# Kernel optimization log

Measured on AMD Instinct MI355X. Metric: run time of the kernel, lower is better.

The kernel has to match this reference:

```python
import jax, jax.numpy as jnp
import numpy as np

INPUT, HIDDEN, OUTPUT = 128, 256, 128
BATCH, SEQ = 128, 2048


def setup_inputs() -> dict:
    key = jax.random.key(0)
    ks = jax.random.split(key, 6)
    s_in = 1.0 / np.sqrt(INPUT)
    s_h = 1.0 / np.sqrt(HIDDEN)
    return {
        "x": jax.random.normal(ks[0], (BATCH, SEQ, INPUT), dtype=jnp.float32),
        "W_in": jax.random.uniform(ks[1], (HIDDEN, INPUT), jnp.float32, -s_in, s_in),
        "b_in": jax.random.uniform(ks[2], (HIDDEN,), jnp.float32, -s_in, s_in),
        "W_rec": jax.random.uniform(ks[3], (HIDDEN, HIDDEN), jnp.float32, -s_h, s_h),
        "W_out": jax.random.uniform(ks[4], (OUTPUT, HIDDEN), jnp.float32, -s_h, s_h),
        "b_out": jax.random.uniform(ks[5], (OUTPUT,), jnp.float32, -s_h, s_h),
    }


def reference(x, W_in, b_in, W_rec, W_out, b_out):
    # Precompute input projection for all timesteps in one big GEMM: [B,S,H]
    xin = jnp.einsum("bsi,hi->bsh", x, W_in) + b_in

    def step(h, xin_t):
        # h: [B,H]; xin_t: [B,H]
        h_new = jax.nn.sigmoid(xin_t + h @ W_rec.T)
        return h_new, None

    h0 = jnp.zeros((x.shape[0], W_rec.shape[0]), dtype=x.dtype)
    h_final, _ = jax.lax.scan(step, h0, jnp.swapaxes(xin, 0, 1))  # scan over seq
    return h_final @ W_out.T + b_out  # [B, OUTPUT]
```

## Files before the change

### kernel.cpp

```cpp
#include <hip/hip_runtime.h>
#include <hip/hip_bf16.h>


#define BATCH 128
#define SEQ   2048
#define NIN   128
#define NH    256
#define NOUT  128

#define BTILE 16
#define NBLK  (BATCH / BTILE)
#define HPITCH 264
#define XPITCH 136
#define TCHUNK 8
#define LOG2E 1.4426950408889634f

typedef __attribute__((ext_vector_type(8))) short short8;
typedef __attribute__((ext_vector_type(4))) float f32x4;

__device__ __forceinline__ ushort f2bf(float f) {
    union { float f; uint u; } v; v.f = f;
    uint r = v.u + 0x7fffu + ((v.u >> 16) & 1u);
    return (ushort)(r >> 16);
}

__device__ __forceinline__ uint pk_bf16(float a, float b) {
    float2 p; p.x = a; p.y = b;
    __hip_bfloat162 h = __float22bfloat162_rn(p);
    union { __hip_bfloat162 h; uint u; } v; v.h = h; return v.u;
}

__device__ __forceinline__ short8 load_wfrag_s(const float* __restrict__ W, int ld,
                                               int row, int col, float scale) {
    const float4* p = (const float4*)(W + (size_t)row * ld + col);
    float4 a = p[0], b = p[1];
    union { short8 v; ushort u[8]; } r;
    r.u[0] = f2bf(a.x * scale); r.u[1] = f2bf(a.y * scale);
    r.u[2] = f2bf(a.z * scale); r.u[3] = f2bf(a.w * scale);
    r.u[4] = f2bf(b.x * scale); r.u[5] = f2bf(b.y * scale);
    r.u[6] = f2bf(b.z * scale); r.u[7] = f2bf(b.w * scale);
    return r.v;
}

__device__ __forceinline__ float bfhi2f(uint u) {
    union { uint u; float f; } v; v.u = u & 0xffff0000u; return v.f;
}
__device__ __forceinline__ float bflo2f(uint u) {
    union { uint u; float f; } v; v.u = u << 16; return v.f;
}

__global__ __launch_bounds__(256, 2)
void xin_gemm(const float* __restrict__ x,
              const float* __restrict__ W_in,
              const float* __restrict__ b_in,
              uint2* __restrict__ xin) {
    const int tid  = threadIdx.x;
    const int lane = tid & 63;
    const int wid  = tid >> 6;
    const int n15  = lane & 15;
    const int q    = lane >> 4;
    const int bblk = blockIdx.x * BTILE;
    const int t0   = blockIdx.y * TCHUNK;

    short8 win[4][4];
    float  bias[4][4];
    #pragma unroll
    for (int mt = 0; mt < 4; ++mt) {
        const int row = (wid * 4 + mt) * 16 + n15;
        #pragma unroll
        for (int kt = 0; kt < 4; ++kt)
            win[mt][kt] = load_wfrag_s(W_in, NIN, row, kt * 32 + q * 8, LOG2E);
        #pragma unroll
        for (int r = 0; r < 4; ++r)
            bias[mt][r] = LOG2E * b_in[(wid * 4 + mt) * 16 + q * 4 + r];
    }

    const float* xrow = x + ((size_t)(bblk + n15) * SEQ + t0) * NIN + q * 8;

    #pragma unroll 1
    for (int tt = 0; tt < TCHUNK; ++tt) {
        const float* xp = xrow + (size_t)tt * NIN;
        short8 bx[4];
        #pragma unroll
        for (int kt = 0; kt < 4; ++kt) {
            const float4* p = (const float4*)(xp + kt * 32);
            float4 a = p[0], b = p[1];
            union { short8 v; uint u[4]; } r;
            r.u[0] = pk_bf16(a.x, a.y);
            r.u[1] = pk_bf16(a.z, a.w);
            r.u[2] = pk_bf16(b.x, b.y);
            r.u[3] = pk_bf16(b.z, b.w);
            bx[kt] = r.v;
        }
        f32x4 acc[4];
        #pragma unroll
        for (int mt = 0; mt < 4; ++mt) {
            acc[mt][0] = bias[mt][0]; acc[mt][1] = bias[mt][1];
            acc[mt][2] = bias[mt][2]; acc[mt][3] = bias[mt][3];
        }
        #pragma unroll
        for (int kt = 0; kt < 4; ++kt)
            #pragma unroll
            for (int mt = 0; mt < 4; ++mt)
                acc[mt] = __builtin_amdgcn_mfma_f32_16x16x32_bf16(
                    win[mt][kt], bx[kt], acc[mt], 0, 0, 0);

        const uint tb = ((uint)(t0 + tt) * NBLK + blockIdx.x) * 16u;
        #pragma unroll
        for (int mt = 0; mt < 4; ++mt) {
            uint2 w;
            w.x = pk_bf16(acc[mt][0], acc[mt][1]);
            w.y = pk_bf16(acc[mt][2], acc[mt][3]);
            xin[(size_t)((tb + wid * 4 + mt) * 64u + lane)] = w;
        }
    }
}

__global__ __launch_bounds__(512, 2)
void elman_scan(const uint2* __restrict__ xin,
                const float* __restrict__ W_rec,
                const float* __restrict__ W_out,
                const float* __restrict__ b_out,
                float* __restrict__ out) {
    const int tid  = threadIdx.x;
    const int lane = tid & 63;
    const int wid  = tid >> 6;
    const int n15  = lane & 15;
    const int q    = lane >> 4;
    const int bblk = blockIdx.x * BTILE;

    __shared__ __align__(16) uint2 hlds[2][16 * 64];

    short8 wrec[2][8];
    #pragma unroll
    for (int mt = 0; mt < 2; ++mt) {
        const int row = (wid * 2 + mt) * 16 + n15;
        #pragma unroll
        for (int kt = 0; kt < 8; ++kt)
            wrec[mt][kt] = load_wfrag_s(W_rec, NH, row, kt * 32 + q * 8, LOG2E);
    }

    for (int i = tid; i < 16 * 64; i += 512) {
        uint2 z; z.x = 0u; z.y = 0u;
        hlds[0][i] = z;
    }

    const uint loff = (uint)blockIdx.x * 1024u + (uint)(wid * 2) * 64u + (uint)lane;

    uint2 xa[2], xb[2];
    #pragma unroll
    for (int mt = 0; mt < 2; ++mt) xa[mt] = xin[(size_t)(loff + mt * 64u)];
    #pragma unroll
    for (int mt = 0; mt < 2; ++mt) xb[mt] = xin[(size_t)(8192u + loff + mt * 64u)];

    __syncthreads();

    const int rbase = n15 * 4 + 2 * (q & 1);
    const int shalf = q >> 1;
    const int woff  = n15 * 4 + q;

    auto step = [&](int t, uint2 (&X)[2]) {
        const int cur = t & 1, nxt = cur ^ 1;

        short8 bh[8];
        #pragma unroll
        for (int kt = 0; kt < 8; ++kt)
            bh[kt] = *(const short8*)&hlds[cur][(2 * kt + shalf) * 64 + rbase];

        f32x4 acc[2];
        #pragma unroll
        for (int mt = 0; mt < 2; ++mt) {
            acc[mt][0] = bflo2f(X[mt].x);
            acc[mt][1] = bfhi2f(X[mt].x);
            acc[mt][2] = bflo2f(X[mt].y);
            acc[mt][3] = bfhi2f(X[mt].y);
        }

        {
            const uint tp = (uint)((t + 2 < SEQ) ? (t + 2) : (SEQ - 1));
            const uint tb = tp * 8192u + loff;
            #pragma unroll
            for (int mt = 0; mt < 2; ++mt) X[mt] = xin[(size_t)(tb + mt * 64u)];
        }

        __builtin_amdgcn_s_setprio(1);
        #pragma unroll
        for (int kt = 0; kt < 8; ++kt)
            #pragma unroll
            for (int mt = 0; mt < 2; ++mt)
                acc[mt] = __builtin_amdgcn_mfma_f32_16x16x32_bf16(
                    wrec[mt][kt], bh[kt], acc[mt], 0, 0, 0);
        __builtin_amdgcn_s_setprio(0);

        #pragma unroll
        for (int mt = 0; mt < 2; ++mt) {
            float h0 = __builtin_amdgcn_rcpf(1.0f + __builtin_amdgcn_exp2f(-acc[mt][0]));
            float h1 = __builtin_amdgcn_rcpf(1.0f + __builtin_amdgcn_exp2f(-acc[mt][1]));
            float h2 = __builtin_amdgcn_rcpf(1.0f + __builtin_amdgcn_exp2f(-acc[mt][2]));
            float h3 = __builtin_amdgcn_rcpf(1.0f + __builtin_amdgcn_exp2f(-acc[mt][3]));
            uint2 w;
            w.x = pk_bf16(h0, h1);
            w.y = pk_bf16(h2, h3);
            hlds[nxt][(wid * 2 + mt) * 64 + woff] = w;
        }

        asm volatile("s_waitcnt lgkmcnt(0)" ::: "memory");
        __builtin_amdgcn_s_barrier();
    };

    #pragma unroll 1
    for (int t = 0; t < SEQ; t += 2) {
        step(t, xa);
        step(t + 1, xb);
    }

    short8 wout[8];
    float  bo[4];
    {
        const int row = wid * 16 + n15;
        #pragma unroll
        for (int kt = 0; kt < 8; ++kt)
            wout[kt] = load_wfrag_s(W_out, NH, row, kt * 32 + q * 8, 1.0f);
        #pragma unroll
        for (int r = 0; r < 4; ++r)
            bo[r] = b_out[wid * 16 + q * 4 + r];
    }
    f32x4 oacc;
    oacc[0] = bo[0]; oacc[1] = bo[1]; oacc[2] = bo[2]; oacc[3] = bo[3];
    #pragma unroll
    for (int kt = 0; kt < 8; ++kt) {
        short8 bh = *(const short8*)&hlds[0][(2 * kt + shalf) * 64 + rbase];
        oacc = __builtin_amdgcn_mfma_f32_16x16x32_bf16(wout[kt], bh, oacc, 0, 0, 0);
    }
    #pragma unroll
    for (int r = 0; r < 4; ++r) {
        const int o = wid * 16 + q * 4 + r;
        out[(size_t)(bblk + n15) * NOUT + o] = oacc[r];
    }
}

__global__ __launch_bounds__(256, 1)
void elman_mfma(const float* __restrict__ x,
                const float* __restrict__ W_in,
                const float* __restrict__ b_in,
                const float* __restrict__ W_rec,
                const float* __restrict__ W_out,
                const float* __restrict__ b_out,
                float* __restrict__ out) {
    const int tid  = threadIdx.x;
    const int lane = tid & 63;
    const int wid  = tid >> 6;
    const int n15  = lane & 15;
    const int q    = lane >> 4;
    const int bblk = blockIdx.x * BTILE;

    __shared__ __align__(16) ushort hlds[2][BTILE * HPITCH];
    __shared__ __align__(16) ushort xlds[2][BTILE * XPITCH];

    short8 wrec[4][8];
    short8 win[4][4];
    float  bias[4][4];
    #pragma unroll
    for (int mt = 0; mt < 4; ++mt) {
        const int row = (wid * 4 + mt) * 16 + n15;
        #pragma unroll
        for (int kt = 0; kt < 8; ++kt)
            wrec[mt][kt] = load_wfrag_s(W_rec, NH, row, kt * 32 + q * 8, 1.0f);
        #pragma unroll
        for (int kt = 0; kt < 4; ++kt)
            win[mt][kt] = load_wfrag_s(W_in, NIN, row, kt * 32 + q * 8, 1.0f);
        #pragma unroll
        for (int r = 0; r < 4; ++r)
            bias[mt][r] = b_in[(wid * 4 + mt) * 16 + q * 4 + r];
    }

    for (int i = tid; i < BTILE * HPITCH / 2; i += 256)
        ((uint*)hlds[0])[i] = 0u;

    const int xr = tid >> 4;
    const int xc = (tid & 15) * 8;
    const size_t xbase = ((size_t)(bblk + xr)) * SEQ * NIN + xc;
    {
        const float4* p = (const float4*)(x + xbase);
        float4 a = p[0], b = p[1];
        union { uint4 u4; ushort s[8]; } px;
        px.s[0] = f2bf(a.x); px.s[1] = f2bf(a.y); px.s[2] = f2bf(a.z); px.s[3] = f2bf(a.w);
        px.s[4] = f2bf(b.x); px.s[5] = f2bf(b.y); px.s[6] = f2bf(b.z); px.s[7] = f2bf(b.w);
        *(uint4*)&xlds[0][xr * XPITCH + xc] = px.u4;
    }
    __syncthreads();

    #pragma unroll 1
    for (int t = 0; t < SEQ; ++t) {
        const int cur = t & 1, nxt = cur ^ 1;
        float4 xp0{}, xp1{};
        if (t + 1 < SEQ) {
            const float4* p = (const float4*)(x + xbase + (size_t)(t + 1) * NIN);
            xp0 = p[0]; xp1 = p[1];
        }
        short8 bx[4], bh[8];
        #pragma unroll
        for (int kt = 0; kt < 4; ++kt)
            bx[kt] = *(const short8*)&xlds[cur][n15 * XPITCH + kt * 32 + q * 8];
        #pragma unroll
        for (int kt = 0; kt < 8; ++kt)
            bh[kt] = *(const short8*)&hlds[cur][n15 * HPITCH + kt * 32 + q * 8];
        f32x4 acc[4];
        #pragma unroll
        for (int mt = 0; mt < 4; ++mt) {
            acc[mt][0] = bias[mt][0]; acc[mt][1] = bias[mt][1];
            acc[mt][2] = bias[mt][2]; acc[mt][3] = bias[mt][3];
        }
        #pragma unroll
        for (int kt = 0; kt < 4; ++kt)
            #pragma unroll
            for (int mt = 0; mt < 4; ++mt)
                acc[mt] = __builtin_amdgcn_mfma_f32_16x16x32_bf16(
                    win[mt][kt], bx[kt], acc[mt], 0, 0, 0);
        #pragma unroll
        for (int kt = 0; kt < 8; ++kt)
            #pragma unroll
            for (int mt = 0; mt < 4; ++mt)
                acc[mt] = __builtin_amdgcn_mfma_f32_16x16x32_bf16(
                    wrec[mt][kt], bh[kt], acc[mt], 0, 0, 0);
        #pragma unroll
        for (int mt = 0; mt < 4; ++mt) {
            float h0 = 1.0f / (1.0f + __expf(-acc[mt][0]));
            float h1 = 1.0f / (1.0f + __expf(-acc[mt][1]));
            float h2 = 1.0f / (1.0f + __expf(-acc[mt][2]));
            float h3 = 1.0f / (1.0f + __expf(-acc[mt][3]));
            uint2 w;
            w.x = pk_bf16(h0, h1);
            w.y = pk_bf16(h2, h3);
            *(uint2*)&hlds[nxt][n15 * HPITCH + (wid * 4 + mt) * 16 + q * 4] = w;
        }
        if (t + 1 < SEQ) {
            union { uint4 u4; ushort s[8]; } px;
            px.s[0] = f2bf(xp0.x); px.s[1] = f2bf(xp0.y);
            px.s[2] = f2bf(xp0.z); px.s[3] = f2bf(xp0.w);
            px.s[4] = f2bf(xp1.x); px.s[5] = f2bf(xp1.y);
            px.s[6] = f2bf(xp1.z); px.s[7] = f2bf(xp1.w);
            *(uint4*)&xlds[nxt][xr * XPITCH + xc] = px.u4;
        }
        __syncthreads();
    }

    short8 wout[2][8];
    float  bo[2][4];
    #pragma unroll
    for (int mo = 0; mo < 2; ++mo) {
        const int row = (wid * 2 + mo) * 16 + n15;
        #pragma unroll
        for (int kt = 0; kt < 8; ++kt)
            wout[mo][kt] = load_wfrag_s(W_out, NH, row, kt * 32 + q * 8, 1.0f);
        #pragma unroll
        for (int r = 0; r < 4; ++r)
            bo[mo][r] = b_out[(wid * 2 + mo) * 16 + q * 4 + r];
    }
    f32x4 oacc[2];
    #pragma unroll
    for (int mo = 0; mo < 2; ++mo) {
        oacc[mo][0] = bo[mo][0]; oacc[mo][1] = bo[mo][1];
        oacc[mo][2] = bo[mo][2]; oacc[mo][3] = bo[mo][3];
    }
    #pragma unroll
    for (int kt = 0; kt < 8; ++kt) {
        short8 bh = *(const short8*)&hlds[0][n15 * HPITCH + kt * 32 + q * 8];
        #pragma unroll
        for (int mo = 0; mo < 2; ++mo)
            oacc[mo] = __builtin_amdgcn_mfma_f32_16x16x32_bf16(
                wout[mo][kt], bh, oacc[mo], 0, 0, 0);
    }
    #pragma unroll
    for (int mo = 0; mo < 2; ++mo)
        #pragma unroll
        for (int r = 0; r < 4; ++r) {
            const int o = (wid * 2 + mo) * 16 + q * 4 + r;
            out[(size_t)(bblk + n15) * NOUT + o] = oacc[mo][r];
        }
}

extern "C" void kernel_launch(void* const* d_in, const int* in_sizes, int n_in,
                              void* d_out, int out_size, void* d_ws, size_t ws_size,
                              hipStream_t stream) {
    const float* x     = (const float*)d_in[0];
    const float* W_in  = (const float*)d_in[1];
    const float* b_in  = (const float*)d_in[2];
    const float* W_rec = (const float*)d_in[3];
    const float* W_out = (const float*)d_in[4];
    const float* b_out = (const float*)d_in[5];
    float* out = (float*)d_out;

    const size_t need = (size_t)SEQ * BATCH * NH * sizeof(ushort);
    if (ws_size >= need) {
        uint2* xin = (uint2*)d_ws;
        dim3 g1(NBLK, SEQ / TCHUNK);
        xin_gemm<<<g1, 256, 0, stream>>>(x, W_in, b_in, xin);
        elman_scan<<<NBLK, 512, 0, stream>>>(xin, W_rec, W_out, b_out, out);
    } else {
        elman_mfma<<<NBLK, 256, 0, stream>>>(x, W_in, b_in, W_rec, W_out, b_out, out);
    }
}
```

Before: 1.351 ms.

## Fuse input projection into recurrent scan kernel with software-pipelined x loads

Removes the separate input-projection GEMM kernel and its bf16 workspace round trip. Each scan step now computes the next timestep's W_in·x projection with MFMAs alongside the recurrent MFMAs, with x prefetched from global memory several steps ahead. This is meant to hide the projection work inside the latency-bound serial scan that uses only a few blocks. In exchange, each sequential step carries extra MFMA work and global load latency, and the fallback kernel is deleted.

After: 3.691 ms. 173% more time.

```diff
diff --git a/kernel.cpp b/kernel.cpp
--- a/kernel.cpp
+++ b/kernel.cpp
@@ -10,9 +10,6 @@
 
 #define BTILE 16
 #define NBLK  (BATCH / BTILE)
-#define HPITCH 264
-#define XPITCH 136
-#define TCHUNK 8
 #define LOG2E 1.4426950408889634f
 
 typedef __attribute__((ext_vector_type(8))) short short8;
@@ -42,102 +39,38 @@
     return r.v;
 }
 
-__device__ __forceinline__ float bfhi2f(uint u) {
-    union { uint u; float f; } v; v.u = u & 0xffff0000u; return v.f;
-}
-__device__ __forceinline__ float bflo2f(uint u) {
-    union { uint u; float f; } v; v.u = u << 16; return v.f;
-}
-
-__global__ __launch_bounds__(256, 2)
-void xin_gemm(const float* __restrict__ x,
-              const float* __restrict__ W_in,
-              const float* __restrict__ b_in,
-              uint2* __restrict__ xin) {
+__global__ __launch_bounds__(512, 2)
+void elman_fused(const float* __restrict__ x,
+                 const float* __restrict__ W_in,
+                 const float* __restrict__ b_in,
+                 const float* __restrict__ W_rec,
+                 const float* __restrict__ W_out,
+                 const float* __restrict__ b_out,
+                 float* __restrict__ out) {
     const int tid  = threadIdx.x;
     const int lane = tid & 63;
     const int wid  = tid >> 6;
     const int n15  = lane & 15;
     const int q    = lane >> 4;
     const int bblk = blockIdx.x * BTILE;
-    const int t0   = blockIdx.y * TCHUNK;
-
-    short8 win[4][4];
-    float  bias[4][4];
-    #pragma unroll
-    for (int mt = 0; mt < 4; ++mt) {
-        const int row = (wid * 4 + mt) * 16 + n15;
+
+    __shared__ __align__(16) uint2 hlds[2][16 * 64];
+
+    short8 wrec[2][8];
+    short8 win[2][4];
+    f32x4  bias[2];
+    #pragma unroll
+    for (int mt = 0; mt < 2; ++mt) {
+        const int row = (wid * 2 + mt) * 16 + n15;
+        #pragma unroll
+        for (int kt = 0; kt < 8; ++kt)
+            wrec[mt][kt] = load_wfrag_s(W_rec, NH, row, kt * 32 + q * 8, LOG2E);
         #pragma unroll
         for (int kt = 0; kt < 4; ++kt)
             win[mt][kt] = load_wfrag_s(W_in, NIN, row, kt * 32 + q * 8, LOG2E);
         #pragma unroll
         for (int r = 0; r < 4; ++r)
-            bias[mt][r] = LOG2E * b_in[(wid * 4 + mt) * 16 + q * 4 + r];
-    }
-
-    const float* xrow = x + ((size_t)(bblk + n15) * SEQ + t0) * NIN + q * 8;
-
-    #pragma unroll 1
-    for (int tt = 0; tt < TCHUNK; ++tt) {
-        const float* xp = xrow + (size_t)tt * NIN;
-        short8 bx[4];
-        #pragma unroll
-        for (int kt = 0; kt < 4; ++kt) {
-            const float4* p = (const float4*)(xp + kt * 32);
-            float4 a = p[0], b = p[1];
-            union { short8 v; uint u[4]; } r;
-            r.u[0] = pk_bf16(a.x, a.y);
-            r.u[1] = pk_bf16(a.z, a.w);
-            r.u[2] = pk_bf16(b.x, b.y);
-            r.u[3] = pk_bf16(b.z, b.w);
-            bx[kt] = r.v;
-        }
-        f32x4 acc[4];
-        #pragma unroll
-        for (int mt = 0; mt < 4; ++mt) {
-            acc[mt][0] = bias[mt][0]; acc[mt][1] = bias[mt][1];
-            acc[mt][2] = bias[mt][2]; acc[mt][3] = bias[mt][3];
-        }
-        #pragma unroll
-        for (int kt = 0; kt < 4; ++kt)
-            #pragma unroll
-            for (int mt = 0; mt < 4; ++mt)
-                acc[mt] = __builtin_amdgcn_mfma_f32_16x16x32_bf16(
-                    win[mt][kt], bx[kt], acc[mt], 0, 0, 0);
-
-        const uint tb = ((uint)(t0 + tt) * NBLK + blockIdx.x) * 16u;
-        #pragma unroll
-        for (int mt = 0; mt < 4; ++mt) {
-            uint2 w;
-            w.x = pk_bf16(acc[mt][0], acc[mt][1]);
-            w.y = pk_bf16(acc[mt][2], acc[mt][3]);
-            xin[(size_t)((tb + wid * 4 + mt) * 64u + lane)] = w;
-        }
-    }
-}
-
-__global__ __launch_bounds__(512, 2)
-void elman_scan(const uint2* __restrict__ xin,
-                const float* __restrict__ W_rec,
-                const float* __restrict__ W_out,
-                const float* __restrict__ b_out,
-                float* __restrict__ out) {
-    const int tid  = threadIdx.x;
-    const int lane = tid & 63;
-    const int wid  = tid >> 6;
-    const int n15  = lane & 15;
-    const int q    = lane >> 4;
-    const int bblk = blockIdx.x * BTILE;
-
-    __shared__ __align__(16) uint2 hlds[2][16 * 64];
-
-    short8 wrec[2][8];
-    #pragma unroll
-    for (int mt = 0; mt < 2; ++mt) {
-        const int row = (wid * 2 + mt) * 16 + n15;
-        #pragma unroll
-        for (int kt = 0; kt < 8; ++kt)
-            wrec[mt][kt] = load_wfrag_s(W_rec, NH, row, kt * 32 + q * 8, LOG2E);
+            bias[mt][r] = LOG2E * b_in[(wid * 2 + mt) * 16 + q * 4 + r];
     }
 
     for (int i = tid; i < 16 * 64; i += 512) {
@@ -145,13 +78,45 @@
         hlds[0][i] = z;
     }
 
-    const uint loff = (uint)blockIdx.x * 1024u + (uint)(wid * 2) * 64u + (uint)lane;
-
-    uint2 xa[2], xb[2];
-    #pragma unroll
-    for (int mt = 0; mt < 2; ++mt) xa[mt] = xin[(size_t)(loff + mt * 64u)];
-    #pragma unroll
-    for (int mt = 0; mt < 2; ++mt) xb[mt] = xin[(size_t)(8192u + loff + mt * 64u)];
+    const float* xrow = x + (size_t)(bblk + n15) * SEQ * NIN + q * 8;
+
+    float4 xr[4][2];
+    short8 bx0[4], bx1[4];
+
+    auto xload = [&](int t) {
+        const float* xp = xrow + (size_t)t * NIN;
+        #pragma unroll
+        for (int kt = 0; kt < 4; ++kt) {
+            const float4* p = (const float4*)(xp + kt * 32);
+            xr[kt][0] = p[0];
+            xr[kt][1] = p[1];
+        }
+    };
+    auto xcvt = [&](short8 (&dst)[4]) {
+        #pragma unroll
+        for (int kt = 0; kt < 4; ++kt) {
+            union { short8 v; uint u[4]; } r;
+            r.u[0] = pk_bf16(xr[kt][0].x, xr[kt][0].y);
+            r.u[1] = pk_bf16(xr[kt][0].z, xr[kt][0].w);
+            r.u[2] = pk_bf16(xr[kt][1].x, xr[kt][1].y);
+            r.u[3] = pk_bf16(xr[kt][1].z, xr[kt][1].w);
+            dst[kt] = r.v;
+        }
+    };
+
+    f32x4 accA[2], accB[2];
+
+    xload(0); xcvt(bx0);
+    #pragma unroll
+    for (int mt = 0; mt < 2; ++mt) accA[mt] = bias[mt];
+    #pragma unroll
+    for (int kt = 0; kt < 4; ++kt)
+        #pragma unroll
+        for (int mt = 0; mt < 2; ++mt)
+            accA[mt] = __builtin_amdgcn_mfma_f32_16x16x32_bf16(
+                win[mt][kt], bx0[kt], accA[mt], 0, 0, 0);
+    xload(1); xcvt(bx1);
+    xload(2);
 
     __syncthreads();
 
@@ -159,7 +124,8 @@
     const int shalf = q >> 1;
     const int woff  = n15 * 4 + q;
 
-    auto step = [&](int t, uint2 (&X)[2]) {
+    auto step = [&](int t, f32x4 (&acc)[2], f32x4 (&accN)[2],
+                    short8 (&bxc)[4], short8 (&bxf)[4]) {
         const int cur = t & 1, nxt = cur ^ 1;
 
         short8 bh[8];
@@ -167,23 +133,16 @@
         for (int kt = 0; kt < 8; ++kt)
             bh[kt] = *(const short8*)&hlds[cur][(2 * kt + shalf) * 64 + rbase];
 
-        f32x4 acc[2];
-        #pragma unroll
-        for (int mt = 0; mt < 2; ++mt) {
-            acc[mt][0] = bflo2f(X[mt].x);
-            acc[mt][1] = bfhi2f(X[mt].x);
-            acc[mt][2] = bflo2f(X[mt].y);
-            acc[mt][3] = bfhi2f(X[mt].y);
-        }
-
-        {
-            const uint tp = (uint)((t + 2 < SEQ) ? (t + 2) : (SEQ - 1));
-            const uint tb = tp * 8192u + loff;
+        __builtin_amdgcn_s_setprio(1);
+        #pragma unroll
+        for (int mt = 0; mt < 2; ++mt) accN[mt] = bias[mt];
+        #pragma unroll
+        for (int kt = 0; kt < 4; ++kt)
             #pragma unroll
-            for (int mt = 0; mt < 2; ++mt) X[mt] = xin[(size_t)(tb + mt * 64u)];
-        }
-
-        __builtin_amdgcn_s_setprio(1);
+            for (int mt = 0; mt < 2; ++mt)
+                accN[mt] = __builtin_amdgcn_mfma_f32_16x16x32_bf16(
+                    win[mt][kt], bxc[kt], accN[mt], 0, 0, 0);
+
         #pragma unroll
         for (int kt = 0; kt < 8; ++kt)
             #pragma unroll
@@ -191,6 +150,12 @@
                 acc[mt] = __builtin_amdgcn_mfma_f32_16x16x32_bf16(
                     wrec[mt][kt], bh[kt], acc[mt], 0, 0, 0);
         __builtin_amdgcn_s_setprio(0);
+
+        xcvt(bxf);
+        {
+            const int tf = (t + 3 < SEQ) ? (t + 3) : (SEQ - 1);
+            xload(tf);
+        }
 
         #pragma unroll
         for (int mt = 0; mt < 2; ++mt) {
@@ -210,8 +175,8 @@
 
     #pragma unroll 1
     for (int t = 0; t < SEQ; t += 2) {
-        step(t, xa);
-        step(t + 1, xb);
+        step(t,     accA, accB, bx1, bx0);
+        step(t + 1, accB, accA, bx0, bx1);
     }
 
     short8 wout[8];
@@ -237,147 +202,6 @@
         const int o = wid * 16 + q * 4 + r;
         out[(size_t)(bblk + n15) * NOUT + o] = oacc[r];
     }
-}
-
-__global__ __launch_bounds__(256, 1)
-void elman_mfma(const float* __restrict__ x,
-                const float* __restrict__ W_in,
-                const float* __restrict__ b_in,
-                const float* __restrict__ W_rec,
-                const float* __restrict__ W_out,
-                const float* __restrict__ b_out,
-                float* __restrict__ out) {
-    const int tid  = threadIdx.x;
-    const int lane = tid & 63;
-    const int wid  = tid >> 6;
-    const int n15  = lane & 15;
-    const int q    = lane >> 4;
-    const int bblk = blockIdx.x * BTILE;
-
-    __shared__ __align__(16) ushort hlds[2][BTILE * HPITCH];
-    __shared__ __align__(16) ushort xlds[2][BTILE * XPITCH];
-
-    short8 wrec[4][8];
-    short8 win[4][4];
-    float  bias[4][4];
-    #pragma unroll
-    for (int mt = 0; mt < 4; ++mt) {
-        const int row = (wid * 4 + mt) * 16 + n15;
-        #pragma unroll
-        for (int kt = 0; kt < 8; ++kt)
-            wrec[mt][kt] = load_wfrag_s(W_rec, NH, row, kt * 32 + q * 8, 1.0f);
-        #pragma unroll
-        for (int kt = 0; kt < 4; ++kt)
-            win[mt][kt] = load_wfrag_s(W_in, NIN, row, kt * 32 + q * 8, 1.0f);
-        #pragma unroll
-        for (int r = 0; r < 4; ++r)
-            bias[mt][r] = b_in[(wid * 4 + mt) * 16 + q * 4 + r];
-    }
-
-    for (int i = tid; i < BTILE * HPITCH / 2; i += 256)
-        ((uint*)hlds[0])[i] = 0u;
-
-    const int xr = tid >> 4;
-    const int xc = (tid & 15) * 8;
-    const size_t xbase = ((size_t)(bblk + xr)) * SEQ * NIN + xc;
-    {
-        const float4* p = (const float4*)(x + xbase);
-        float4 a = p[0], b = p[1];
-        union { uint4 u4; ushort s[8]; } px;
-        px.s[0] = f2bf(a.x); px.s[1] = f2bf(a.y); px.s[2] = f2bf(a.z); px.s[3] = f2bf(a.w);
-        px.s[4] = f2bf(b.x); px.s[5] = f2bf(b.y); px.s[6] = f2bf(b.z); px.s[7] = f2bf(b.w);
-        *(uint4*)&xlds[0][xr * XPITCH + xc] = px.u4;
-    }
-    __syncthreads();
-
-    #pragma unroll 1
-    for (int t = 0; t < SEQ; ++t) {
-        const int cur = t & 1, nxt = cur ^ 1;
-        float4 xp0{}, xp1{};
-        if (t + 1 < SEQ) {
-            const float4* p = (const float4*)(x + xbase + (size_t)(t + 1) * NIN);
-            xp0 = p[0]; xp1 = p[1];
-        }
-        short8 bx[4], bh[8];
-        #pragma unroll
-        for (int kt = 0; kt < 4; ++kt)
-            bx[kt] = *(const short8*)&xlds[cur][n15 * XPITCH + kt * 32 + q * 8];
-        #pragma unroll
-        for (int kt = 0; kt < 8; ++kt)
-            bh[kt] = *(const short8*)&hlds[cur][n15 * HPITCH + kt * 32 + q * 8];
-        f32x4 acc[4];
-        #pragma unroll
-        for (int mt = 0; mt < 4; ++mt) {
-            acc[mt][0] = bias[mt][0]; acc[mt][1] = bias[mt][1];
-            acc[mt][2] = bias[mt][2]; acc[mt][3] = bias[mt][3];
-        }
-        #pragma unroll
-        for (int kt = 0; kt < 4; ++kt)
-            #pragma unroll
-            for (int mt = 0; mt < 4; ++mt)
-                acc[mt] = __builtin_amdgcn_mfma_f32_16x16x32_bf16(
-                    win[mt][kt], bx[kt], acc[mt], 0, 0, 0);
-        #pragma unroll
-        for (int kt = 0; kt < 8; ++kt)
-            #pragma unroll
-            for (int mt = 0; mt < 4; ++mt)
-                acc[mt] = __builtin_amdgcn_mfma_f32_16x16x32_bf16(
-                    wrec[mt][kt], bh[kt], acc[mt], 0, 0, 0);
-        #pragma unroll
-        for (int mt = 0; mt < 4; ++mt) {
-            float h0 = 1.0f / (1.0f + __expf(-acc[mt][0]));
-            float h1 = 1.0f / (1.0f + __expf(-acc[mt][1]));
-            float h2 = 1.0f / (1.0f + __expf(-acc[mt][2]));
-            float h3 = 1.0f / (1.0f + __expf(-acc[mt][3]));
-            uint2 w;
-            w.x = pk_bf16(h0, h1);
-            w.y = pk_bf16(h2, h3);
-            *(uint2*)&hlds[nxt][n15 * HPITCH + (wid * 4 + mt) * 16 + q * 4] = w;
-        }
-        if (t + 1 < SEQ) {
-            union { uint4 u4; ushort s[8]; } px;
-            px.s[0] = f2bf(xp0.x); px.s[1] = f2bf(xp0.y);
-            px.s[2] = f2bf(xp0.z); px.s[3] = f2bf(xp0.w);
-            px.s[4] = f2bf(xp1.x); px.s[5] = f2bf(xp1.y);
-            px.s[6] = f2bf(xp1.z); px.s[7] = f2bf(xp1.w);
-            *(uint4*)&xlds[nxt][xr * XPITCH + xc] = px.u4;
-        }
-        __syncthreads();
-    }
-
-    short8 wout[2][8];
-    float  bo[2][4];
-    #pragma unroll
-    for (int mo = 0; mo < 2; ++mo) {
-        const int row = (wid * 2 + mo) * 16 + n15;
-        #pragma unroll
-        for (int kt = 0; kt < 8; ++kt)
-            wout[mo][kt] = load_wfrag_s(W_out, NH, row, kt * 32 + q * 8, 1.0f);
-        #pragma unroll
-        for (int r = 0; r < 4; ++r)
-            bo[mo][r] = b_out[(wid * 2 + mo) * 16 + q * 4 + r];
-    }
-    f32x4 oacc[2];
-    #pragma unroll
-    for (int mo = 0; mo < 2; ++mo) {
-        oacc[mo][0] = bo[mo][0]; oacc[mo][1] = bo[mo][1];
-        oacc[mo][2] = bo[mo][2]; oacc[mo][3] = bo[mo][3];
-    }
-    #pragma unroll
-    for (int kt = 0; kt < 8; ++kt) {
-        short8 bh = *(const short8*)&hlds[0][n15 * HPITCH + kt * 32 + q * 8];
-        #pragma unroll
-        for (int mo = 0; mo < 2; ++mo)
-            oacc[mo] = __builtin_amdgcn_mfma_f32_16x16x32_bf16(
-                wout[mo][kt], bh, oacc[mo], 0, 0, 0);
-    }
-    #pragma unroll
-    for (int mo = 0; mo < 2; ++mo)
-        #pragma unroll
-        for (int r = 0; r < 4; ++r) {
-            const int o = (wid * 2 + mo) * 16 + q * 4 + r;
-            out[(size_t)(bblk + n15) * NOUT + o] = oacc[mo][r];
-        }
 }
 
 extern "C" void kernel_launch(void* const* d_in, const int* in_sizes, int n_in,
@@ -391,13 +215,5 @@
     const float* b_out = (const float*)d_in[5];
     float* out = (float*)d_out;
 
-    const size_t need = (size_t)SEQ * BATCH * NH * sizeof(ushort);
-    if (ws_size >= need) {
-        uint2* xin = (uint2*)d_ws;
-        dim3 g1(NBLK, SEQ / TCHUNK);
-        xin_gemm<<<g1, 256, 0, stream>>>(x, W_in, b_in, xin);
-        elman_scan<<<NBLK, 512, 0, stream>>>(xin, W_rec, W_out, b_out, out);
-    } else {
-        elman_mfma<<<NBLK, 256, 0, stream>>>(x, W_in, b_in, W_rec, W_out, b_out, out);
-    }
-}
+    elman_fused<<<NBLK, 512, 0, stream>>>(x, W_in, b_in, W_rec, W_out, b_out, out);
+}
```

## Fuse input-projection GEMM and recurrent scan into one kernel with flag-based handoff

Applied to the files above, without the earlier changes.

Merges the separate xin GEMM and scan kernels into a single launch. The first 8 blocks run the recurrence while the remaining blocks compute 8-timestep chunks of the input projection and publish per-chunk release flags, which the scan blocks acquire-wait on before consuming each chunk. This overlaps the projection with the serial scan and drops the second kernel launch. It relies on the producer blocks being scheduled while the scan blocks spin, relies on a large dynamic shared-memory request that limits occupancy, adds a memset, and removes the no-workspace fallback path.

Result: slower. 1.438 ms (+6.4%).

```diff
diff --git a/kernel.cpp b/kernel.cpp
--- a/kernel.cpp
+++ b/kernel.cpp
@@ -10,10 +10,11 @@
 
 #define BTILE 16
 #define NBLK  (BATCH / BTILE)
+#define TCHUNK 8
+#define NCHUNK (SEQ / TCHUNK)
+#define LOG2E 1.4426950408889634f
 #define HPITCH 264
 #define XPITCH 136
-#define TCHUNK 8
-#define LOG2E 1.4426950408889634f
 
 typedef __attribute__((ext_vector_type(8))) short short8;
 typedef __attribute__((ext_vector_type(4))) float f32x4;
@@ -47,6 +48,220 @@
 }
 __device__ __forceinline__ float bflo2f(uint u) {
     union { uint u; float f; } v; v.u = u << 16; return v.f;
+}
+
+__global__ __launch_bounds__(512, 2)
+void elman_fused(const float* __restrict__ x,
+                 const float* __restrict__ W_in,
+                 const float* __restrict__ b_in,
+                 const float* __restrict__ W_rec,
+                 const float* __restrict__ W_out,
+                 const float* __restrict__ b_out,
+                 float* __restrict__ out,
+                 uint2* __restrict__ xin,
+                 uint*  __restrict__ flags) {
+    const int tid  = threadIdx.x;
+    const int lane = tid & 63;
+    const int wid  = tid >> 6;
+    const int n15  = lane & 15;
+    const int q    = lane >> 4;
+
+    __shared__ __align__(16) uint2 hlds[2][16 * 64];
+
+    if (blockIdx.x >= NBLK) {
+        const int pid  = blockIdx.x - NBLK;
+        const int c    = pid >> 3;
+        const int b    = pid & 7;
+        const int bblk = b * BTILE;
+        const int t0   = c * TCHUNK;
+
+        short8 win[2][4];
+        float  bias[2][4];
+        #pragma unroll
+        for (int mt = 0; mt < 2; ++mt) {
+            const int row = (wid * 2 + mt) * 16 + n15;
+            #pragma unroll
+            for (int kt = 0; kt < 4; ++kt)
+                win[mt][kt] = load_wfrag_s(W_in, NIN, row, kt * 32 + q * 8, LOG2E);
+            #pragma unroll
+            for (int r = 0; r < 4; ++r)
+                bias[mt][r] = LOG2E * b_in[(wid * 2 + mt) * 16 + q * 4 + r];
+        }
+
+        const float* xrow = x + ((size_t)(bblk + n15) * SEQ + t0) * NIN + q * 8;
+
+        #pragma unroll 1
+        for (int tt = 0; tt < TCHUNK; ++tt) {
+            const float* xp = xrow + (size_t)tt * NIN;
+            short8 bx[4];
+            #pragma unroll
+            for (int kt = 0; kt < 4; ++kt) {
+                const float4* p = (const float4*)(xp + kt * 32);
+                float4 a = p[0], bb = p[1];
+                union { short8 v; uint u[4]; } r;
+                r.u[0] = pk_bf16(a.x, a.y);
+                r.u[1] = pk_bf16(a.z, a.w);
+                r.u[2] = pk_bf16(bb.x, bb.y);
+                r.u[3] = pk_bf16(bb.z, bb.w);
+                bx[kt] = r.v;
+            }
+            f32x4 acc[2];
+            #pragma unroll
+            for (int mt = 0; mt < 2; ++mt) {
+                acc[mt][0] = bias[mt][0]; acc[mt][1] = bias[mt][1];
+                acc[mt][2] = bias[mt][2]; acc[mt][3] = bias[mt][3];
+            }
+            #pragma unroll
+            for (int kt = 0; kt < 4; ++kt)
+                #pragma unroll
+                for (int mt = 0; mt < 2; ++mt)
+                    acc[mt] = __builtin_amdgcn_mfma_f32_16x16x32_bf16(
+                        win[mt][kt], bx[kt], acc[mt], 0, 0, 0);
+
+            const uint tb = ((uint)(t0 + tt) * NBLK + (uint)b) * 16u;
+            #pragma unroll
+            for (int mt = 0; mt < 2; ++mt) {
+                uint2 w;
+                w.x = pk_bf16(acc[mt][0], acc[mt][1]);
+                w.y = pk_bf16(acc[mt][2], acc[mt][3]);
+                xin[(size_t)((tb + wid * 2 + mt) * 64u + lane)] = w;
+            }
+        }
+
+        __syncthreads();
+        if (tid == 0) {
+            __threadfence();
+            __hip_atomic_store(&flags[b * NCHUNK + c], 1u,
+                               __ATOMIC_RELEASE, __HIP_MEMORY_SCOPE_AGENT);
+        }
+        return;
+    }
+
+    const int  bblk  = blockIdx.x * BTILE;
+    const uint fbase = (uint)blockIdx.x * NCHUNK;
+
+    short8 wrec[2][8];
+    #pragma unroll
+    for (int mt = 0; mt < 2; ++mt) {
+        const int row = (wid * 2 + mt) * 16 + n15;
+        #pragma unroll
+        for (int kt = 0; kt < 8; ++kt)
+            wrec[mt][kt] = load_wfrag_s(W_rec, NH, row, kt * 32 + q * 8, LOG2E);
+    }
+
+    for (int i = tid; i < 16 * 64; i += 512) {
+        uint2 z; z.x = 0u; z.y = 0u;
+        hlds[0][i] = z;
+    }
+
+    const uint loff = (uint)blockIdx.x * 1024u + (uint)(wid * 2) * 64u + (uint)lane;
+
+    auto gate = [&](int cc) {
+        if (tid == 0) {
+            while (__hip_atomic_load(&flags[fbase + (uint)cc],
+                                     __ATOMIC_ACQUIRE, __HIP_MEMORY_SCOPE_AGENT) == 0u)
+                __builtin_amdgcn_s_sleep(8);
+        }
+        __syncthreads();
+        __builtin_amdgcn_fence(__ATOMIC_ACQUIRE, "agent");
+    };
+
+    gate(0);
+
+    uint2 xa[2], xb[2];
+    #pragma unroll
+    for (int mt = 0; mt < 2; ++mt) xa[mt] = xin[(size_t)(loff + mt * 64u)];
+    #pragma unroll
+    for (int mt = 0; mt < 2; ++mt) xb[mt] = xin[(size_t)(8192u + loff + mt * 64u)];
+
+    __syncthreads();
+
+    const int rbase = n15 * 4 + 2 * (q & 1);
+    const int shalf = q >> 1;
+    const int woff  = n15 * 4 + q;
+
+    auto step = [&](int t, uint2 (&X)[2]) {
+        const int cur = t & 1, nxt = cur ^ 1;
+
+        short8 bh[8];
+        #pragma unroll
+        for (int kt = 0; kt < 8; ++kt)
+            bh[kt] = *(const short8*)&hlds[cur][(2 * kt + shalf) * 64 + rbase];
+
+        f32x4 acc[2];
+        #pragma unroll
+        for (int mt = 0; mt < 2; ++mt) {
+            acc[mt][0] = bflo2f(X[mt].x);
+            acc[mt][1] = bfhi2f(X[mt].x);
+            acc[mt][2] = bflo2f(X[mt].y);
+            acc[mt][3] = bfhi2f(X[mt].y);
+        }
+
+        {
+            const uint tp = (uint)((t + 2 < SEQ) ? (t + 2) : (SEQ - 1));
+            const uint tb = tp * 8192u + loff;
+            #pragma unroll
+            for (int mt = 0; mt < 2; ++mt) X[mt] = xin[(size_t)(tb + mt * 64u)];
+        }
+
+        __builtin_amdgcn_s_setprio(1);
+        #pragma unroll
+        for (int kt = 0; kt < 8; ++kt)
+            #pragma unroll
+            for (int mt = 0; mt < 2; ++mt)
+                acc[mt] = __builtin_amdgcn_mfma_f32_16x16x32_bf16(
+                    wrec[mt][kt], bh[kt], acc[mt], 0, 0, 0);
+        __builtin_amdgcn_s_setprio(0);
+
+        #pragma unroll
+        for (int mt = 0; mt < 2; ++mt) {
+            float h0 = __builtin_amdgcn_rcpf(1.0f + __builtin_amdgcn_exp2f(-acc[mt][0]));
+            float h1 = __builtin_amdgcn_rcpf(1.0f + __builtin_amdgcn_exp2f(-acc[mt][1]));
+            float h2 = __builtin_amdgcn_rcpf(1.0f + __builtin_amdgcn_exp2f(-acc[mt][2]));
+            float h3 = __builtin_amdgcn_rcpf(1.0f + __builtin_amdgcn_exp2f(-acc[mt][3]));
+            uint2 w;
+            w.x = pk_bf16(h0, h1);
+            w.y = pk_bf16(h2, h3);
+            hlds[nxt][(wid * 2 + mt) * 64 + woff] = w;
+        }
+
+        asm volatile("s_waitcnt lgkmcnt(0)" ::: "memory");
+        __builtin_amdgcn_s_barrier();
+    };
+
+    #pragma unroll 1
+    for (int t = 0; t < SEQ; t += 2) {
+        if ((t & 7) == 0) {
+            const int cc = (t >> 3) + 1;
+            gate(cc < NCHUNK ? cc : NCHUNK - 1);
+        }
+        step(t, xa);
+        step(t + 1, xb);
+    }
+
+    short8 wout[8];
+    float  bo[4];
+    {
+        const int row = wid * 16 + n15;
+        #pragma unroll
+        for (int kt = 0; kt < 8; ++kt)
+            wout[kt] = load_wfrag_s(W_out, NH, row, kt * 32 + q * 8, 1.0f);
+        #pragma unroll
+        for (int r = 0; r < 4; ++r)
+            bo[r] = b_out[wid * 16 + q * 4 + r];
+    }
+    f32x4 oacc;
+    oacc[0] = bo[0]; oacc[1] = bo[1]; oacc[2] = bo[2]; oacc[3] = bo[3];
+    #pragma unroll
+    for (int kt = 0; kt < 8; ++kt) {
+        short8 bh = *(const short8*)&hlds[0][(2 * kt + shalf) * 64 + rbase];
+        oacc = __builtin_amdgcn_mfma_f32_16x16x32_bf16(wout[kt], bh, oacc, 0, 0, 0);
+    }
+    #pragma unroll
+    for (int r = 0; r < 4; ++r) {
+        const int o = wid * 16 + q * 4 + r;
+        out[(size_t)(bblk + n15) * NOUT + o] = oacc[r];
+    }
 }
 
 __global__ __launch_bounds__(256, 2)
@@ -161,12 +376,10 @@
 
     auto step = [&](int t, uint2 (&X)[2]) {
         const int cur = t & 1, nxt = cur ^ 1;
-
         short8 bh[8];
         #pragma unroll
         for (int kt = 0; kt < 8; ++kt)
             bh[kt] = *(const short8*)&hlds[cur][(2 * kt + shalf) * 64 + rbase];
-
         f32x4 acc[2];
         #pragma unroll
         for (int mt = 0; mt < 2; ++mt) {
@@ -175,14 +388,12 @@
             acc[mt][2] = bflo2f(X[mt].y);
             acc[mt][3] = bfhi2f(X[mt].y);
         }
-
         {
             const uint tp = (uint)((t + 2 < SEQ) ? (t + 2) : (SEQ - 1));
             const uint tb = tp * 8192u + loff;
             #pragma unroll
             for (int mt = 0; mt < 2; ++mt) X[mt] = xin[(size_t)(tb + mt * 64u)];
         }
-
         __builtin_amdgcn_s_setprio(1);
         #pragma unroll
         for (int kt = 0; kt < 8; ++kt)
@@ -191,7 +402,6 @@
                 acc[mt] = __builtin_amdgcn_mfma_f32_16x16x32_bf16(
                     wrec[mt][kt], bh[kt], acc[mt], 0, 0, 0);
         __builtin_amdgcn_s_setprio(0);
-
         #pragma unroll
         for (int mt = 0; mt < 2; ++mt) {
             float h0 = __builtin_amdgcn_rcpf(1.0f + __builtin_amdgcn_exp2f(-acc[mt][0]));
@@ -203,7 +413,6 @@
             w.y = pk_bf16(h2, h3);
             hlds[nxt][(wid * 2 + mt) * 64 + woff] = w;
         }
-
         asm volatile("s_waitcnt lgkmcnt(0)" ::: "memory");
         __builtin_amdgcn_s_barrier();
     };
@@ -237,147 +446,6 @@
         const int o = wid * 16 + q * 4 + r;
         out[(size_t)(bblk + n15) * NOUT + o] = oacc[r];
     }
-}
-
-__global__ __launch_bounds__(256, 1)
-void elman_mfma(const float* __restrict__ x,
-                const float* __restrict__ W_in,
-                const float* __restrict__ b_in,
-                const float* __restrict__ W_rec,
-                const float* __restrict__ W_out,
-                const float* __restrict__ b_out,
-                float* __restrict__ out) {
-    const int tid  = threadIdx.x;
-    const int lane = tid & 63;
-    const int wid  = tid >> 6;
-    const int n15  = lane & 15;
-    const int q    = lane >> 4;
-    const int bblk = blockIdx.x * BTILE;
-
-    __shared__ __align__(16) ushort hlds[2][BTILE * HPITCH];
-    __shared__ __align__(16) ushort xlds[2][BTILE * XPITCH];
-
-    short8 wrec[4][8];
-    short8 win[4][4];
-    float  bias[4][4];
-    #pragma unroll
-    for (int mt = 0; mt < 4; ++mt) {
-        const int row = (wid * 4 + mt) * 16 + n15;
-        #pragma unroll
-        for (int kt = 0; kt < 8; ++kt)
-            wrec[mt][kt] = load_wfrag_s(W_rec, NH, row, kt * 32 + q * 8, 1.0f);
-        #pragma unroll
-        for (int kt = 0; kt < 4; ++kt)
-            win[mt][kt] = load_wfrag_s(W_in, NIN, row, kt * 32 + q * 8, 1.0f);
-        #pragma unroll
-        for (int r = 0; r < 4; ++r)
-            bias[mt][r] = b_in[(wid * 4 + mt) * 16 + q * 4 + r];
-    }
-
-    for (int i = tid; i < BTILE * HPITCH / 2; i += 256)
-        ((uint*)hlds[0])[i] = 0u;
-
-    const int xr = tid >> 4;
-    const int xc = (tid & 15) * 8;
-    const size_t xbase = ((size_t)(bblk + xr)) * SEQ * NIN + xc;
-    {
-        const float4* p = (const float4*)(x + xbase);
-        float4 a = p[0], b = p[1];
-        union { uint4 u4; ushort s[8]; } px;
-        px.s[0] = f2bf(a.x); px.s[1] = f2bf(a.y); px.s[2] = f2bf(a.z); px.s[3] = f2bf(a.w);
-        px.s[4] = f2bf(b.x); px.s[5] = f2bf(b.y); px.s[6] = f2bf(b.z); px.s[7] = f2bf(b.w);
-        *(uint4*)&xlds[0][xr * XPITCH + xc] = px.u4;
-    }
-    __syncthreads();
-
-    #pragma unroll 1
-    for (int t = 0; t < SEQ; ++t) {
-        const int cur = t & 1, nxt = cur ^ 1;
-        float4 xp0{}, xp1{};
-        if (t + 1 < SEQ) {
-            const float4* p = (const float4*)(x + xbase + (size_t)(t + 1) * NIN);
-            xp0 = p[0]; xp1 = p[1];
-        }
-        short8 bx[4], bh[8];
-        #pragma unroll
-        for (int kt = 0; kt < 4; ++kt)
-            bx[kt] = *(const short8*)&xlds[cur][n15 * XPITCH + kt * 32 + q * 8];
-        #pragma unroll
-        for (int kt = 0; kt < 8; ++kt)
-            bh[kt] = *(const short8*)&hlds[cur][n15 * HPITCH + kt * 32 + q * 8];
-        f32x4 acc[4];
-        #pragma unroll
-        for (int mt = 0; mt < 4; ++mt) {
-            acc[mt][0] = bias[mt][0]; acc[mt][1] = bias[mt][1];
-            acc[mt][2] = bias[mt][2]; acc[mt][3] = bias[mt][3];
-        }
-        #pragma unroll
-        for (int kt = 0; kt < 4; ++kt)
-            #pragma unroll
-            for (int mt = 0; mt < 4; ++mt)
-                acc[mt] = __builtin_amdgcn_mfma_f32_16x16x32_bf16(
-                    win[mt][kt], bx[kt], acc[mt], 0, 0, 0);
-        #pragma unroll
-        for (int kt = 0; kt < 8; ++kt)
-            #pragma unroll
-            for (int mt = 0; mt < 4; ++mt)
-                acc[mt] = __builtin_amdgcn_mfma_f32_16x16x32_bf16(
-                    wrec[mt][kt], bh[kt], acc[mt], 0, 0, 0);
-        #pragma unroll
-        for (int mt = 0; mt < 4; ++mt) {
-            float h0 = 1.0f / (1.0f + __expf(-acc[mt][0]));
-            float h1 = 1.0f / (1.0f + __expf(-acc[mt][1]));
-            float h2 = 1.0f / (1.0f + __expf(-acc[mt][2]));
-            float h3 = 1.0f / (1.0f + __expf(-acc[mt][3]));
-            uint2 w;
-            w.x = pk_bf16(h0, h1);
-            w.y = pk_bf16(h2, h3);
-            *(uint2*)&hlds[nxt][n15 * HPITCH + (wid * 4 + mt) * 16 + q * 4] = w;
-        }
-        if (t + 1 < SEQ) {
-            union { uint4 u4; ushort s[8]; } px;
-            px.s[0] = f2bf(xp0.x); px.s[1] = f2bf(xp0.y);
-            px.s[2] = f2bf(xp0.z); px.s[3] = f2bf(xp0.w);
-            px.s[4] = f2bf(xp1.x); px.s[5] = f2bf(xp1.y);
-            px.s[6] = f2bf(xp1.z); px.s[7] = f2bf(xp1.w);
-            *(uint4*)&xlds[nxt][xr * XPITCH + xc] = px.u4;
-        }
-        __syncthreads();
-    }
-
-    short8 wout[2][8];
-    float  bo[2][4];
-    #pragma unroll
-    for (int mo = 0; mo < 2; ++mo) {
-        const int row = (wid * 2 + mo) * 16 + n15;
-        #pragma unroll
-        for (int kt = 0; kt < 8; ++kt)
-            wout[mo][kt] = load_wfrag_s(W_out, NH, row, kt * 32 + q * 8, 1.0f);
-        #pragma unroll
-        for (int r = 0; r < 4; ++r)
-            bo[mo][r] = b_out[(wid * 2 + mo) * 16 + q * 4 + r];
-    }
-    f32x4 oacc[2];
-    #pragma unroll
-    for (int mo = 0; mo < 2; ++mo) {
-        oacc[mo][0] = bo[mo][0]; oacc[mo][1] = bo[mo][1];
-        oacc[mo][2] = bo[mo][2]; oacc[mo][3] = bo[mo][3];
-    }
-    #pragma unroll
-    for (int kt = 0; kt < 8; ++kt) {
-        short8 bh = *(const short8*)&hlds[0][n15 * HPITCH + kt * 32 + q * 8];
-        #pragma unroll
-        for (int mo = 0; mo < 2; ++mo)
-            oacc[mo] = __builtin_amdgcn_mfma_f32_16x16x32_bf16(
-                wout[mo][kt], bh, oacc[mo], 0, 0, 0);
-    }
-    #pragma unroll
-    for (int mo = 0; mo < 2; ++mo)
-        #pragma unroll
-        for (int r = 0; r < 4; ++r) {
-            const int o = (wid * 2 + mo) * 16 + q * 4 + r;
-            out[(size_t)(bblk + n15) * NOUT + o] = oacc[mo][r];
-        }
 }
 
 extern "C" void kernel_launch(void* const* d_in, const int* in_sizes, int n_in,
@@ -391,13 +459,19 @@
     const float* b_out = (const float*)d_in[5];
     float* out = (float*)d_out;
 
-    const size_t need = (size_t)SEQ * BATCH * NH * sizeof(ushort);
-    if (ws_size >= need) {
+    const size_t xin_bytes  = (size_t)SEQ * BATCH * NH * sizeof(ushort);
+    const size_t flag_bytes = (size_t)NBLK * NCHUNK * sizeof(uint);
+
+    if (ws_size >= xin_bytes + flag_bytes) {
+        uint2* xin  = (uint2*)d_ws;
+        uint* flags = (uint*)((char*)d_ws + xin_bytes);
+        hipMemsetAsync(flags, 0, flag_bytes, stream);
+        elman_fused<<<NBLK + NBLK * NCHUNK, 512, 96 * 1024, stream>>>(
+            x, W_in, b_in, W_rec, W_out, b_out, out, xin, flags);
+    } else if (ws_size >= xin_bytes) {
         uint2* xin = (uint2*)d_ws;
         dim3 g1(NBLK, SEQ / TCHUNK);
         xin_gemm<<<g1, 256, 0, stream>>>(x, W_in, b_in, xin);
         elman_scan<<<NBLK, 512, 0, stream>>>(xin, W_rec, W_out, b_out, out);
-    } else {
-        elman_mfma<<<NBLK, 256, 0, stream>>>(x, W_in, b_in, W_rec, W_out, b_out, out);
-    }
-}
+    }
+}
```
